# Performance work log

Measured on AMD Instinct MI355X. Metric: run time of the kernel, lower is better.

The kernel has to match this reference:

```python
import jax, jax.numpy as jnp
import numpy as np

N_NODES = 50000
N_RAND_EDGES = 800000
NEG_SLOPE = 0.2


def gat_conv(h, src, dst, W, attn_l, attn_r, bias, res_W=None, act=False):
    # DGL GATConv semantics: fc -> per-node attn halves -> per-edge leaky_relu
    # logits -> segment softmax over destination -> weighted scatter-sum.
    N = h.shape[0]
    H, D = attn_l.shape
    feat = (h @ W).reshape(N, H, D)                      # (N,H,D)
    el = (feat * attn_l[None]).sum(-1)                   # (N,H)
    er = (feat * attn_r[None]).sum(-1)                   # (N,H)
    e = jax.nn.leaky_relu(el[src] + er[dst], NEG_SLOPE)  # (E,H)
    emax = jax.ops.segment_max(e, dst, num_segments=N)   # (N,H)
    ee = jnp.exp(e - emax[dst])                          # (E,H)
    denom = jax.ops.segment_sum(ee, dst, num_segments=N)
    alpha = ee / denom[dst]                              # (E,H)
    msg = feat[src] * alpha[:, :, None]                  # (E,H,D) dominant traffic
    rst = jax.ops.segment_sum(msg, dst, num_segments=N)  # (N,H,D)
    if res_W is not None:
        rst = rst + (h @ res_W).reshape(N, H, D)
    rst = rst + bias.reshape(1, H, D)
    if act:
        rst = jax.nn.relu(rst)
    return rst


def setup_inputs() -> dict:
    key = jax.random.key(0)
    ks = jax.random.split(key, 20)
    x = jax.random.normal(ks[0], (N_NODES, 64), dtype=jnp.float32)
    src_r = jax.random.randint(ks[1], (N_RAND_EDGES,), 0, N_NODES, dtype=jnp.int32)
    dst_r = jax.random.randint(ks[2], (N_RAND_EDGES,), 0, N_NODES, dtype=jnp.int32)
    loops = jnp.arange(N_NODES, dtype=jnp.int32)
    src = jnp.concatenate([src_r, loops])   # self-loops: no zero in-degree
    dst = jnp.concatenate([dst_r, loops])
    s = 0.1
    p = lambda k, shp: jax.random.normal(k, shp, dtype=jnp.float32) * s
    return {
        "x": x, "src": src, "dst": dst,
        # layer 1: in=64 -> hid=32, heads=4, relu, no residual
        "W1": p(ks[3], (64, 128)), "al1": p(ks[4], (4, 32)), "ar1": p(ks[5], (4, 32)),
        "b1": jnp.zeros((128,), jnp.float32),
        # layer 2: in=128 -> hid=32, heads=4, relu, residual
        "W2": p(ks[6], (128, 128)), "al2": p(ks[7], (4, 32)), "ar2": p(ks[8], (4, 32)),
        "b2": jnp.zeros((128,), jnp.float32), "resW2": p(ks[9], (128, 128)),
        # layer 3: in=128 -> out=1, heads=6, no activation, residual
        "W3": p(ks[10], (128, 6)), "al3": p(ks[11], (6, 1)), "ar3": p(ks[12], (6, 1)),
        "b3": jnp.zeros((6,), jnp.float32), "resW3": p(ks[13], (128, 6)),
    }


def reference(x, src, dst, W1, al1, ar1, b1, W2, al2, ar2, b2, resW2,
              W3, al3, ar3, b3, resW3):
    h = gat_conv(x, src, dst, W1, al1, ar1, b1, None, act=True)
    h = h.reshape(h.shape[0], -1)                        # flatten heads
    h = gat_conv(h, src, dst, W2, al2, ar2, b2, resW2, act=True)
    h = h.reshape(h.shape[0], -1)
    h = gat_conv(h, src, dst, W3, al3, ar3, b3, resW3, act=False)
    return h.mean(axis=1)                                # mean over heads -> (N, out)
```

## Files before the change

### kernel.cpp

```cpp
#include <hip/hip_runtime.h>
#include <hip/hip_fp16.h>

#define NEG 0.2f
#define BUCKET_SHIFT 7
#define CAP 3200
#define PCHUNK 4096

typedef _Float16 h8 __attribute__((ext_vector_type(8)));
typedef float f4v __attribute__((ext_vector_type(4)));


__device__ __forceinline__ void wconv_dev(int bid, const float* __restrict__ W2,
                                          const float* __restrict__ rW2,
                                          float4* __restrict__ W2f,
                                          float4* __restrict__ rW2f) {
    int c = bid * 256 + threadIdx.x;
    int which = c >> 11;
    int cc = c & 2047;
    int kb = cc >> 9, rem = cc & 511, t = rem >> 6, lane = rem & 63;
    int n = (t << 4) + (lane & 15);
    int k0 = (kb << 5) + ((lane >> 4) << 3);
    const float* S = which ? rW2 : W2;
    h8 v;
#pragma unroll
    for (int i = 0; i < 8; i++) v[i] = (_Float16)S[(k0 + i) * 128 + n];
    ((h8*)(which ? rW2f : W2f))[cc] = v;
}

__device__ __forceinline__ void partition_dev(char* smem, int bid,
                                              const int* __restrict__ src,
                                              const int* __restrict__ dst,
                                              int* __restrict__ cursor,
                                              unsigned* __restrict__ part,
                                              int E, int NB) {
    unsigned* stash = (unsigned*)smem;
    int* hist = (int*)(smem + PCHUNK * 4);
    int* base = hist + 512;
    const int tid = threadIdx.x;
    const int e0 = bid * PCHUNK;

    for (int i = tid; i < NB; i += 256) hist[i] = 0;
    __syncthreads();

    for (int i = tid; i < PCHUNK; i += 256) {
        int e = e0 + i;
        unsigned pk = 0xFFFFFFFFu;
        if (e < E) {
            int d = dst[e];
            pk = ((unsigned)d << 16) | (unsigned)src[e];
            atomicAdd(&hist[d >> BUCKET_SHIFT], 1);
        }
        stash[i] = pk;
    }
    __syncthreads();

    for (int i = tid; i < NB; i += 256) {
        int hcnt = hist[i];
        base[i] = hcnt ? atomicAdd(&cursor[i], hcnt) : 0;
        hist[i] = 0;
    }
    __syncthreads();

    for (int i = tid; i < PCHUNK; i += 256) {
        unsigned pk = stash[i];
        if (pk != 0xFFFFFFFFu) {
            int b = pk >> (16 + BUCKET_SHIFT);
            int r = base[b] + atomicAdd(&hist[b], 1);
            if (r < CAP) part[(size_t)b * CAP + r] = pk;
        }
    }
}

__device__ __forceinline__ void bucket_dev(char* smem, int b,
                                           const int* __restrict__ cursor,
                                           const unsigned* __restrict__ part,
                                           int* __restrict__ csr_src,
                                           int* __restrict__ row_beg,
                                           int* __restrict__ row_end, int N) {
    int* cnt = (int*)smem;
    int* sc = cnt + 128;
    int* ex = sc + 128;
    int* cur = ex + 128;
    int* lcsr = cur + 128;
    const int tid = threadIdx.x;
    int m = cursor[b];
    m = m < CAP ? m : CAP;
    if (tid < 128) cnt[tid] = 0;
    __syncthreads();

    const unsigned* pp = part + (size_t)b * CAP;
    for (int i = tid; i < m; i += 256) atomicAdd(&cnt[(pp[i] >> 16) & 127], 1);
    __syncthreads();

    if (tid < 128) sc[tid] = cnt[tid];
    __syncthreads();
    for (int off = 1; off < 128; off <<= 1) {
        int t = (tid < 128 && tid >= off) ? sc[tid - off] : 0;
        __syncthreads();
        if (tid < 128) sc[tid] += t;
        __syncthreads();
    }
    if (tid < 128) {
        ex[tid] = sc[tid] - cnt[tid];
        cur[tid] = 0;
    }
    __syncthreads();

    for (int i = tid; i < m; i += 256) {
        unsigned pk = pp[i];
        int dlo = (pk >> 16) & 127;
        int r = atomicAdd(&cur[dlo], 1);
        lcsr[ex[dlo] + r] = (int)(pk & 0xFFFFu);
    }
    __syncthreads();

    const int gbase = b * CAP;
    for (int i = tid; i < m; i += 256) csr_src[gbase + i] = lcsr[i];
    int n = (b << BUCKET_SHIFT) + tid;
    if (tid < 128 && n < N) {
        row_beg[n] = gbase + ex[tid];
        row_end[n] = gbase + sc[tid];
    }
}

__device__ __forceinline__ void gemm_el_dev(char* smem, int bid,
                                            const float* __restrict__ A,
                                            const float* __restrict__ W,
                                            const float* __restrict__ al,
                                            const float* __restrict__ ar,
                                            __half* __restrict__ feat_h,
                                            float* __restrict__ el,
                                            float* __restrict__ er, int N) {
    constexpr int K = 64;
    float* As = (float*)smem;
    const int c = threadIdx.x & 31;
    const int rg = threadIdx.x >> 5;
    const int row0 = bid << 6;
    const int K4 = K >> 2;

    const float4* Av = (const float4*)A;
    float4* AsV = (float4*)As;
    for (int idx = threadIdx.x; idx < 16 * K; idx += 256) {
        int rr = idx / K4, kk4 = idx - rr * K4;
        int row = row0 + rr;
        float4 v = make_float4(0.f, 0.f, 0.f, 0.f);
        if (row < N) v = Av[(size_t)row * K4 + kk4];
        AsV[rr * K4 + kk4] = v;
    }
    __syncthreads();

    const float4* Wv = (const float4*)W;
    float4 acc[8];
#pragma unroll
    for (int i = 0; i < 8; i++) acc[i] = make_float4(0.f, 0.f, 0.f, 0.f);

    for (int k4 = 0; k4 < K4; k4++) {
        float4 a[8];
#pragma unroll
        for (int i = 0; i < 8; i++) a[i] = AsV[(rg * 8 + i) * K4 + k4];
#pragma unroll
        for (int kk = 0; kk < 4; kk++) {
            float4 w = Wv[((k4 << 2) + kk) * 32 + c];
#pragma unroll
            for (int i = 0; i < 8; i++) {
                float av = kk == 0 ? a[i].x : kk == 1 ? a[i].y : kk == 2 ? a[i].z : a[i].w;
                acc[i].x += av * w.x;
                acc[i].y += av * w.y;
                acc[i].z += av * w.z;
                acc[i].w += av * w.w;
            }
        }
    }

    __half2* Fh2 = (__half2*)feat_h;
#pragma unroll
    for (int i = 0; i < 8; i++) {
        int row = row0 + rg * 8 + i;
        if (row < N) {
            size_t o = ((size_t)row << 6) + (c << 1);
            Fh2[o] = __floats2half2_rn(acc[i].x, acc[i].y);
            Fh2[o + 1] = __floats2half2_rn(acc[i].z, acc[i].w);
        }
    }

    float4 alv = ((const float4*)al)[c];
    float4 arv = ((const float4*)ar)[c];
    float pel[8], per_[8];
#pragma unroll
    for (int i = 0; i < 8; i++) {
        pel[i] = acc[i].x * alv.x + acc[i].y * alv.y + acc[i].z * alv.z + acc[i].w * alv.w;
        per_[i] = acc[i].x * arv.x + acc[i].y * arv.y + acc[i].z * arv.z + acc[i].w * arv.w;
    }
#pragma unroll
    for (int m = 1; m < 8; m <<= 1) {
#pragma unroll
        for (int i = 0; i < 8; i++) {
            pel[i] += __shfl_xor(pel[i], m);
            per_[i] += __shfl_xor(per_[i], m);
        }
    }
    if ((c & 7) == 0) {
        int h = c >> 3;
#pragma unroll
        for (int i = 0; i < 8; i++) {
            int row = row0 + rg * 8 + i;
            if (row < N) {
                el[(row << 2) + h] = pel[i];
                er[(row << 2) + h] = per_[i];
            }
        }
    }
}

__global__ __launch_bounds__(256) void stage1_k(const float* __restrict__ W2,
                                                const float* __restrict__ rW2,
                                                float4* __restrict__ W2f,
                                                float4* __restrict__ rW2f,
                                                const int* __restrict__ src,
                                                const int* __restrict__ dst,
                                                int* __restrict__ cursor,
                                                unsigned* __restrict__ part,
                                                int E, int NB) {
    __shared__ __align__(16) char smem[20480];
    if (blockIdx.x < 16)
        wconv_dev(blockIdx.x, W2, rW2, W2f, rW2f);
    else
        partition_dev(smem, blockIdx.x - 16, src, dst, cursor, part, E, NB);
}

__global__ __launch_bounds__(256) void stage2_k(const int* __restrict__ cursor,
                                                const unsigned* __restrict__ part,
                                                int* __restrict__ csr_src,
                                                int* __restrict__ row_beg,
                                                int* __restrict__ row_end, int NB,
                                                const float* __restrict__ x,
                                                const float* __restrict__ W1,
                                                const float* __restrict__ al1,
                                                const float* __restrict__ ar1,
                                                __half* __restrict__ featA,
                                                float* __restrict__ el,
                                                float* __restrict__ er, int N) {
    __shared__ __align__(16) char smem[16384];
    if ((int)blockIdx.x < NB)
        bucket_dev(smem, blockIdx.x, cursor, part, csr_src, row_beg, row_end, N);
    else
        gemm_el_dev(smem, blockIdx.x - NB, x, W1, al1, ar1, featA, el, er, N);
}

#define MFMA_STAGE_AND_LOOP()                                                   \
    const int tid = threadIdx.x;                                                \
    const int row0 = blockIdx.x << 6;                                           \
    for (int i = tid; i < 2048; i += 256) WsF[i] = Wf[i];                       \
    const float4* Afv = (const float4*)A;                                       \
    for (int idx = tid; idx < 1024; idx += 256) {                               \
        int r = idx >> 4, kc = idx & 15;                                        \
        float4 v = make_float4(0.f, 0.f, 0.f, 0.f);                             \
        int row = row0 + r;                                                     \
        if (row < N) v = Afv[(size_t)row * 16 + kc];                            \
        int d = ((r >> 4) * 4 + (kc >> 2)) * 64 + (kc & 3) * 16 + (r & 15);     \
        AsF[d] = v;                                                             \
    }                                                                           \
    __syncthreads();                                                            \
    const int w = tid >> 6;                                                     \
    const int lane = tid & 63;                                                  \
    const h8* Ah = (const h8*)AsF;                                              \
    const h8* Wh = (const h8*)WsF;                                              \
    f4v acc[8];                                                                 \
    _Pragma("unroll") for (int t = 0; t < 8; t++) acc[t] = (f4v){0.f, 0.f, 0.f, 0.f}; \
    _Pragma("unroll") for (int kb = 0; kb < 4; kb++) {                          \
        h8 af = Ah[(w * 4 + kb) * 64 + lane];                                   \
        _Pragma("unroll") for (int t = 0; t < 8; t++) {                         \
            h8 bf = Wh[(kb * 8 + t) * 64 + lane];                               \
            acc[t] = __builtin_amdgcn_mfma_f32_16x16x32_f16(af, bf, acc[t], 0, 0, 0); \
        }                                                                       \
    }                                                                           \
    const int c16 = lane & 15;                                                  \
    const int rg = lane >> 4;

__global__ __launch_bounds__(256) void mfma_el_k(const _Float16* __restrict__ A,
                                                 const float4* __restrict__ Wf,
                                                 const float* __restrict__ al,
                                                 const float* __restrict__ ar,
                                                 _Float16* __restrict__ feat,
                                                 float* __restrict__ el,
                                                 float* __restrict__ er, int N) {
    __shared__ float4 WsF[2048];
    __shared__ float4 AsF[1024];
    MFMA_STAGE_AND_LOOP()

    float alv[8], arv[8];
#pragma unroll
    for (int t = 0; t < 8; t++) {
        alv[t] = al[(t << 4) + c16];
        arv[t] = ar[(t << 4) + c16];
    }
    float pel[4][4], per_[4][4];
#pragma unroll
    for (int j = 0; j < 4; j++)
#pragma unroll
        for (int hh = 0; hh < 4; hh++) {
            pel[j][hh] = acc[2 * hh][j] * alv[2 * hh] + acc[2 * hh + 1][j] * alv[2 * hh + 1];
            per_[j][hh] = acc[2 * hh][j] * arv[2 * hh] + acc[2 * hh + 1][j] * arv[2 * hh + 1];
        }
#pragma unroll
    for (int m = 1; m < 16; m <<= 1)
#pragma unroll
        for (int j = 0; j < 4; j++)
#pragma unroll
            for (int hh = 0; hh < 4; hh++) {
                pel[j][hh] += __shfl_xor(pel[j][hh], m);
                per_[j][hh] += __shfl_xor(per_[j][hh], m);
            }
    if (c16 == 0) {
#pragma unroll
        for (int j = 0; j < 4; j++) {
            int row = row0 + (w << 4) + (rg << 2) + j;
            if (row < N) {
                ((float4*)el)[row] = make_float4(pel[j][0], pel[j][1], pel[j][2], pel[j][3]);
                ((float4*)er)[row] = make_float4(per_[j][0], per_[j][1], per_[j][2], per_[j][3]);
            }
        }
    }

    _Float16* As2 = (_Float16*)AsF + (w << 11);
#pragma unroll
    for (int t = 0; t < 8; t++)
#pragma unroll
        for (int j = 0; j < 4; j++)
            As2[((rg << 2) + j) * 128 + (t << 4) + c16] = (_Float16)acc[t][j];
    __asm__ volatile("s_waitcnt lgkmcnt(0)" ::: "memory");
    const float4* As2v = (const float4*)As2;
    float4* featv = (float4*)feat;
#pragma unroll
    for (int ii = 0; ii < 4; ii++) {
        int ch = ii * 64 + lane;
        int row = row0 + (w << 4) + (ch >> 4);
        if (row < N) featv[(size_t)row * 16 + (ch & 15)] = As2v[ch];
    }
}

__global__ __launch_bounds__(256) void mfma_res_k(const _Float16* __restrict__ A,
                                                  const float4* __restrict__ Wf,
                                                  const _Float16* __restrict__ rsth,
                                                  const float* __restrict__ b2,
                                                  const float* __restrict__ W3,
                                                  const float* __restrict__ resW3,
                                                  const float* __restrict__ b3,
                                                  float* __restrict__ feat3,
                                                  float* __restrict__ res3, int N) {
    __shared__ float4 WsF[2048];
    __shared__ float4 AsF[1024];
    MFMA_STAGE_AND_LOOP()

    float4* As2v = (float4*)AsF + (w << 8);
#pragma unroll
    for (int ii = 0; ii < 4; ii++) {
        int ch = ii * 64 + lane;
        int row = row0 + (w << 4) + (ch >> 4);
        float4 v = make_float4(0.f, 0.f, 0.f, 0.f);
        if (row < N) v = ((const float4*)rsth)[(size_t)row * 16 + (ch & 15)];
        As2v[ch] = v;
    }
    __asm__ volatile("s_waitcnt lgkmcnt(0)" ::: "memory");
    const _Float16* As2 = (const _Float16*)As2v;

    float b2v[8];
#pragma unroll
    for (int t = 0; t < 8; t++) b2v[t] = b2[(t << 4) + c16];

    float hv[8][4];
#pragma unroll
    for (int t = 0; t < 8; t++)
#pragma unroll
        for (int j = 0; j < 4; j++) {
            float rv = (float)As2[((rg << 2) + j) * 128 + (t << 4) + c16];
            hv[t][j] = fmaxf(acc[t][j] + rv + b2v[t], 0.f);
        }

    float f3[4][6], r3[4][6];
#pragma unroll
    for (int j = 0; j < 4; j++)
#pragma unroll
        for (int h = 0; h < 6; h++) {
            f3[j][h] = 0.f;
            r3[j][h] = 0.f;
        }
#pragma unroll
    for (int t = 0; t < 8; t++) {
        int col = (t << 4) + c16;
        const float* w3p = W3 + col * 6;
        const float* rwp = resW3 + col * 6;
#pragma unroll
        for (int h = 0; h < 6; h++) {
            float w3 = w3p[h], rw = rwp[h];
#pragma unroll
            for (int j = 0; j < 4; j++) {
                f3[j][h] = fmaf(hv[t][j], w3, f3[j][h]);
                r3[j][h] = fmaf(hv[t][j], rw, r3[j][h]);
            }
        }
    }
#pragma unroll
    for (int m = 1; m < 16; m <<= 1)
#pragma unroll
        for (int j = 0; j < 4; j++)
#pragma unroll
            for (int h = 0; h < 6; h++) {
                f3[j][h] += __shfl_xor(f3[j][h], m);
                r3[j][h] += __shfl_xor(r3[j][h], m);
            }
    if (c16 == 0) {
#pragma unroll
        for (int j = 0; j < 4; j++) {
            int row = row0 + (w << 4) + (rg << 2) + j;
            if (row < N) {
#pragma unroll
                for (int h = 0; h < 6; h++) {
                    feat3[row * 6 + h] = f3[j][h];
                    res3[row * 6 + h] = r3[j][h] + b3[h];
                }
            }
        }
    }
}

template <bool BR>
__global__ __launch_bounds__(256) void pull2_k(const int* __restrict__ row_beg,
                                               const int* __restrict__ row_end,
                                               const int* __restrict__ csr_src,
                                               const float* __restrict__ el,
                                               const float* __restrict__ er,
                                               const __half* __restrict__ feat_h,
                                               const float* __restrict__ bias,
                                               __half* __restrict__ outp, int N) {
    int n = (blockIdx.x << 2) + (threadIdx.x >> 6);
    if (n >= N) return;
    unsigned l = threadIdx.x & 63;
    unsigned h = l >> 4;
    float erd = er[((unsigned)n << 2) + h];
    const __half2* feat2 = (const __half2*)feat_h;
    int beg = __builtin_amdgcn_readfirstlane(row_beg[n]);
    int end = __builtin_amdgcn_readfirstlane(row_end[n]);
    float ax = 0.f, ay = 0.f, den = 0.f;
    int p = beg;
    for (; p + 4 <= end; p += 4) {
        int s0 = csr_src[p], s1 = csr_src[p + 1];
        int s2 = csr_src[p + 2], s3 = csr_src[p + 3];
        float e0 = el[((unsigned)s0 << 2) + h];
        float e1 = el[((unsigned)s1 << 2) + h];
        float e2 = el[((unsigned)s2 << 2) + h];
        float e3 = el[((unsigned)s3 << 2) + h];
        __half2 g0 = feat2[((unsigned)s0 << 6) + l];
        __half2 g1 = feat2[((unsigned)s1 << 6) + l];
        __half2 g2 = feat2[((unsigned)s2 << 6) + l];
        __half2 g3 = feat2[((unsigned)s3 << 6) + l];
        float x0 = e0 + erd, x1 = e1 + erd, x2 = e2 + erd, x3 = e3 + erd;
        x0 = fmaxf(x0, NEG * x0);
        x1 = fmaxf(x1, NEG * x1);
        x2 = fmaxf(x2, NEG * x2);
        x3 = fmaxf(x3, NEG * x3);
        float w0 = __expf(x0), w1 = __expf(x1), w2 = __expf(x2), w3 = __expf(x3);
        float2 f0 = __half22float2(g0), f1 = __half22float2(g1);
        float2 f2 = __half22float2(g2), f3 = __half22float2(g3);
        den += (w0 + w1) + (w2 + w3);
        ax = fmaf(w0, f0.x, ax);
        ay = fmaf(w0, f0.y, ay);
        ax = fmaf(w1, f1.x, ax);
        ay = fmaf(w1, f1.y, ay);
        ax = fmaf(w2, f2.x, ax);
        ay = fmaf(w2, f2.y, ay);
        ax = fmaf(w3, f3.x, ax);
        ay = fmaf(w3, f3.y, ay);
    }
    for (; p < end; p++) {
        int s0 = csr_src[p];
        float e0 = el[((unsigned)s0 << 2) + h];
        __half2 g0 = feat2[((unsigned)s0 << 6) + l];
        float x0 = e0 + erd;
        x0 = fmaxf(x0, NEG * x0);
        float w0 = __expf(x0);
        float2 f0 = __half22float2(g0);
        den += w0;
        ax = fmaf(w0, f0.x, ax);
        ay = fmaf(w0, f0.y, ay);
    }
    float inv = 1.f / den;
    float vx = ax * inv, vy = ay * inv;
    if (BR) {
        float2 b = ((const float2*)bias)[l];
        vx = fmaxf(vx + b.x, 0.f);
        vy = fmaxf(vy + b.y, 0.f);
    }
    ((__half2*)outp)[((size_t)n << 6) + l] = __floats2half2_rn(vx, vy);
}

__global__ __launch_bounds__(256) void pull6f_k(const int* __restrict__ row_beg,
                                                const int* __restrict__ row_end,
                                                const int* __restrict__ csr_src,
                                                const float* __restrict__ feat3,
                                                const float* __restrict__ al3,
                                                const float* __restrict__ ar3,
                                                const float* __restrict__ res3,
                                                float* __restrict__ out, int N) {
    int n = blockIdx.x * blockDim.x + threadIdx.x;
    if (n >= N) return;
    float a3[6], fdr[6], acc[6], den[6];
#pragma unroll
    for (int h = 0; h < 6; h++) {
        a3[h] = al3[h];
        fdr[h] = feat3[n * 6 + h] * ar3[h];
        acc[h] = 0.f;
        den[h] = 0.f;
    }
    int beg = row_beg[n], end = row_end[n];
    for (int p = beg; p < end; p++) {
        int s = csr_src[p];
#pragma unroll
        for (int h = 0; h < 6; h++) {
            float f = feat3[(unsigned)s * 6 + h];
            float x = fmaf(f, a3[h], fdr[h]);
            x = fmaxf(x, NEG * x);
            float w = __expf(x);
            den[h] += w;
            acc[h] = fmaf(w, f, acc[h]);
        }
    }
    float m = 0.f;
#pragma unroll
    for (int h = 0; h < 6; h++) m += acc[h] / den[h] + res3[n * 6 + h];
    out[n] = m * (1.f / 6.f);
}

extern "C" void kernel_launch(void* const* d_in, const int* in_sizes, int n_in,
                              void* d_out, int out_size, void* d_ws, size_t ws_size,
                              hipStream_t stream) {
    const float* x = (const float*)d_in[0];
    const int* src = (const int*)d_in[1];
    const int* dst = (const int*)d_in[2];
    const float* W1 = (const float*)d_in[3];
    const float* al1 = (const float*)d_in[4];
    const float* ar1 = (const float*)d_in[5];
    const float* b1 = (const float*)d_in[6];
    const float* W2 = (const float*)d_in[7];
    const float* al2 = (const float*)d_in[8];
    const float* ar2 = (const float*)d_in[9];
    const float* b2 = (const float*)d_in[10];
    const float* resW2 = (const float*)d_in[11];
    const float* W3 = (const float*)d_in[12];
    const float* al3 = (const float*)d_in[13];
    const float* ar3 = (const float*)d_in[14];
    const float* b3 = (const float*)d_in[15];
    const float* resW3 = (const float*)d_in[16];
    float* out = (float*)d_out;

    const int N = in_sizes[0] / 64;
    const int E = in_sizes[1];
    const int NB = (N + 127) >> BUCKET_SHIFT;

    float* ws = (float*)d_ws;
    __half* featA = (__half*)ws;
    __half* h2h = (__half*)(ws + (size_t)N * 64);
    __half* rsth = (__half*)(ws + (size_t)N * 128);
    float* el = ws + (size_t)N * 192;
    float* er = el + (size_t)N * 4;
    float* feat3 = el;
    float* res3 = ws + (size_t)N * 200;
    float* W2f = res3 + (size_t)N * 6;
    float* rW2f = W2f + 8192;
    int* ip = (int*)(rW2f + 8192);
    int* cursor = ip;
    int* row_beg = cursor + 512;
    int* row_end = row_beg + N;
    unsigned* part = (unsigned*)(row_end + N);
    int* csr_src = (int*)(part + (size_t)NB * CAP);

    const int gN = (N + 255) / 256;
    const int gN64 = (N + 63) / 64;
    const int gNw = (N + 3) / 4;
    const int gP = (E + PCHUNK - 1) / PCHUNK;

    hipMemsetAsync(cursor, 0, sizeof(int) * 512, stream);
    stage1_k<<<16 + gP, 256, 0, stream>>>(W2, resW2, (float4*)W2f, (float4*)rW2f,
                                          src, dst, cursor, part, E, NB);
    stage2_k<<<NB + gN64, 256, 0, stream>>>(cursor, part, csr_src, row_beg, row_end,
                                            NB, x, W1, al1, ar1, featA, el, er, N);

    pull2_k<true><<<gNw, 256, 0, stream>>>(row_beg, row_end, csr_src, el, er,
                                           featA, b1, h2h, N);

    mfma_el_k<<<gN64, 256, 0, stream>>>((const _Float16*)h2h, (const float4*)W2f,
                                        al2, ar2, (_Float16*)featA, el, er, N);
    pull2_k<false><<<gNw, 256, 0, stream>>>(row_beg, row_end, csr_src, el, er,
                                            featA, nullptr, rsth, N);
    mfma_res_k<<<gN64, 256, 0, stream>>>((const _Float16*)h2h, (const float4*)rW2f,
                                         (const _Float16*)rsth, b2, W3, resW3, b3,
                                         feat3, res3, N);

    pull6f_k<<<gN, 256, 0, stream>>>(row_beg, row_end, csr_src, feat3, al3, ar3,
                                     res3, out, N);
}
```

Measured before the change: 253.7 us.

## Use half-wave per node with 8-byte gathers; pad layer-3 features for float4 loads

pull2_k now maps each destination node to 32 lanes instead of 64, so one wavefront serves two nodes. Each lane gathers four fp16 features with a single 8-byte load and issues half as many el loads and exp calls per feature, which raises memory-level parallelism. Layer-3 features are stored with a stride of 8 floats so pull6f_k can fetch each source row with two float4 loads instead of six scalar loads. The trade-off is that the two nodes in a wavefront can have different degrees, causing loop divergence, and the row bounds are no longer wave-uniform scalars.

```diff
diff --git a/kernel.cpp b/kernel.cpp
--- a/kernel.cpp
+++ b/kernel.cpp
@@ -416,7 +416,7 @@
             if (row < N) {
 #pragma unroll
                 for (int h = 0; h < 6; h++) {
-                    feat3[row * 6 + h] = f3[j][h];
+                    feat3[(size_t)row * 8 + h] = f3[j][h];
                     res3[row * 6 + h] = r3[j][h] + b3[h];
                 }
             }
@@ -433,15 +433,14 @@
                                                const __half* __restrict__ feat_h,
                                                const float* __restrict__ bias,
                                                __half* __restrict__ outp, int N) {
-    int n = (blockIdx.x << 2) + (threadIdx.x >> 6);
+    int n = (blockIdx.x << 3) + (threadIdx.x >> 5);
     if (n >= N) return;
-    unsigned l = threadIdx.x & 63;
-    unsigned h = l >> 4;
+    unsigned q = threadIdx.x & 31;
+    unsigned h = q >> 3;
     float erd = er[((unsigned)n << 2) + h];
-    const __half2* feat2 = (const __half2*)feat_h;
-    int beg = __builtin_amdgcn_readfirstlane(row_beg[n]);
-    int end = __builtin_amdgcn_readfirstlane(row_end[n]);
-    float ax = 0.f, ay = 0.f, den = 0.f;
+    const uint2* feat4 = (const uint2*)feat_h;
+    int beg = row_beg[n], end = row_end[n];
+    float a0 = 0.f, a1 = 0.f, a2 = 0.f, a3 = 0.f, den = 0.f;
     int p = beg;
     for (; p + 4 <= end; p += 4) {
         int s0 = csr_src[p], s1 = csr_src[p + 1];
@@ -450,48 +449,73 @@
         float e1 = el[((unsigned)s1 << 2) + h];
         float e2 = el[((unsigned)s2 << 2) + h];
         float e3 = el[((unsigned)s3 << 2) + h];
-        __half2 g0 = feat2[((unsigned)s0 << 6) + l];
-        __half2 g1 = feat2[((unsigned)s1 << 6) + l];
-        __half2 g2 = feat2[((unsigned)s2 << 6) + l];
-        __half2 g3 = feat2[((unsigned)s3 << 6) + l];
+        uint2 g0 = feat4[((unsigned)s0 << 5) + q];
+        uint2 g1 = feat4[((unsigned)s1 << 5) + q];
+        uint2 g2 = feat4[((unsigned)s2 << 5) + q];
+        uint2 g3 = feat4[((unsigned)s3 << 5) + q];
         float x0 = e0 + erd, x1 = e1 + erd, x2 = e2 + erd, x3 = e3 + erd;
         x0 = fmaxf(x0, NEG * x0);
         x1 = fmaxf(x1, NEG * x1);
         x2 = fmaxf(x2, NEG * x2);
         x3 = fmaxf(x3, NEG * x3);
         float w0 = __expf(x0), w1 = __expf(x1), w2 = __expf(x2), w3 = __expf(x3);
-        float2 f0 = __half22float2(g0), f1 = __half22float2(g1);
-        float2 f2 = __half22float2(g2), f3 = __half22float2(g3);
         den += (w0 + w1) + (w2 + w3);
-        ax = fmaf(w0, f0.x, ax);
-        ay = fmaf(w0, f0.y, ay);
-        ax = fmaf(w1, f1.x, ax);
-        ay = fmaf(w1, f1.y, ay);
-        ax = fmaf(w2, f2.x, ax);
-        ay = fmaf(w2, f2.y, ay);
-        ax = fmaf(w3, f3.x, ax);
-        ay = fmaf(w3, f3.y, ay);
+        float2 lo, hi;
+        lo = __half22float2(*(__half2*)&g0.x);
+        hi = __half22float2(*(__half2*)&g0.y);
+        a0 = fmaf(w0, lo.x, a0);
+        a1 = fmaf(w0, lo.y, a1);
+        a2 = fmaf(w0, hi.x, a2);
+        a3 = fmaf(w0, hi.y, a3);
+        lo = __half22float2(*(__half2*)&g1.x);
+        hi = __half22float2(*(__half2*)&g1.y);
+        a0 = fmaf(w1, lo.x, a0);
+        a1 = fmaf(w1, lo.y, a1);
+        a2 = fmaf(w1, hi.x, a2);
+        a3 = fmaf(w1, hi.y, a3);
+        lo = __half22float2(*(__half2*)&g2.x);
+        hi = __half22float2(*(__half2*)&g2.y);
+        a0 = fmaf(w2, lo.x, a0);
+        a1 = fmaf(w2, lo.y, a1);
+        a2 = fmaf(w2, hi.x, a2);
+        a3 = fmaf(w2, hi.y, a3);
+        lo = __half22float2(*(__half2*)&g3.x);
+        hi = __half22float2(*(__half2*)&g3.y);
+        a0 = fmaf(w3, lo.x, a0);
+        a1 = fmaf(w3, lo.y, a1);
+        a2 = fmaf(w3, hi.x, a2);
+        a3 = fmaf(w3, hi.y, a3);
     }
     for (; p < end; p++) {
         int s0 = csr_src[p];
         float e0 = el[((unsigned)s0 << 2) + h];
-        __half2 g0 = feat2[((unsigned)s0 << 6) + l];
+        uint2 g0 = feat4[((unsigned)s0 << 5) + q];
         float x0 = e0 + erd;
         x0 = fmaxf(x0, NEG * x0);
         float w0 = __expf(x0);
-        float2 f0 = __half22float2(g0);
         den += w0;
-        ax = fmaf(w0, f0.x, ax);
-        ay = fmaf(w0, f0.y, ay);
+        float2 lo = __half22float2(*(__half2*)&g0.x);
+        float2 hi = __half22float2(*(__half2*)&g0.y);
+        a0 = fmaf(w0, lo.x, a0);
+        a1 = fmaf(w0, lo.y, a1);
+        a2 = fmaf(w0, hi.x, a2);
+        a3 = fmaf(w0, hi.y, a3);
     }
     float inv = 1.f / den;
-    float vx = ax * inv, vy = ay * inv;
+    float v0 = a0 * inv, v1 = a1 * inv, v2 = a2 * inv, v3 = a3 * inv;
     if (BR) {
-        float2 b = ((const float2*)bias)[l];
-        vx = fmaxf(vx + b.x, 0.f);
-        vy = fmaxf(vy + b.y, 0.f);
-    }
-    ((__half2*)outp)[((size_t)n << 6) + l] = __floats2half2_rn(vx, vy);
+        float4 bv = ((const float4*)bias)[q];
+        v0 = fmaxf(v0 + bv.x, 0.f);
+        v1 = fmaxf(v1 + bv.y, 0.f);
+        v2 = fmaxf(v2 + bv.z, 0.f);
+        v3 = fmaxf(v3 + bv.w, 0.f);
+    }
+    __half2 o01 = __floats2half2_rn(v0, v1);
+    __half2 o23 = __floats2half2_rn(v2, v3);
+    uint2 st;
+    st.x = *(unsigned*)&o01;
+    st.y = *(unsigned*)&o23;
+    ((uint2*)outp)[((size_t)n << 5) + q] = st;
 }
 
 __global__ __launch_bounds__(256) void pull6f_k(const int* __restrict__ row_beg,
@@ -504,25 +528,28 @@
                                                 float* __restrict__ out, int N) {
     int n = blockIdx.x * blockDim.x + threadIdx.x;
     if (n >= N) return;
+    const float4* f4p = (const float4*)feat3;
     float a3[6], fdr[6], acc[6], den[6];
 #pragma unroll
     for (int h = 0; h < 6; h++) {
         a3[h] = al3[h];
-        fdr[h] = feat3[n * 6 + h] * ar3[h];
+        fdr[h] = feat3[(size_t)n * 8 + h] * ar3[h];
         acc[h] = 0.f;
         den[h] = 0.f;
     }
     int beg = row_beg[n], end = row_end[n];
     for (int p = beg; p < end; p++) {
         int s = csr_src[p];
+        float4 fa = f4p[(size_t)s * 2];
+        float4 fb = f4p[(size_t)s * 2 + 1];
+        float f[6] = {fa.x, fa.y, fa.z, fa.w, fb.x, fb.y};
 #pragma unroll
         for (int h = 0; h < 6; h++) {
-            float f = feat3[(unsigned)s * 6 + h];
-            float x = fmaf(f, a3[h], fdr[h]);
+            float x = fmaf(f[h], a3[h], fdr[h]);
             x = fmaxf(x, NEG * x);
             float w = __expf(x);
             den[h] += w;
-            acc[h] = fmaf(w, f, acc[h]);
+            acc[h] = fmaf(w, f[h], acc[h]);
         }
     }
     float m = 0.f;
@@ -576,7 +603,7 @@
 
     const int gN = (N + 255) / 256;
     const int gN64 = (N + 63) / 64;
-    const int gNw = (N + 3) / 4;
+    const int gNw8 = (N + 7) / 8;
     const int gP = (E + PCHUNK - 1) / PCHUNK;
 
     hipMemsetAsync(cursor, 0, sizeof(int) * 512, stream);
@@ -585,13 +612,13 @@
     stage2_k<<<NB + gN64, 256, 0, stream>>>(cursor, part, csr_src, row_beg, row_end,
                                             NB, x, W1, al1, ar1, featA, el, er, N);
 
-    pull2_k<true><<<gNw, 256, 0, stream>>>(row_beg, row_end, csr_src, el, er,
-                                           featA, b1, h2h, N);
+    pull2_k<true><<<gNw8, 256, 0, stream>>>(row_beg, row_end, csr_src, el, er,
+                                            featA, b1, h2h, N);
 
     mfma_el_k<<<gN64, 256, 0, stream>>>((const _Float16*)h2h, (const float4*)W2f,
                                         al2, ar2, (_Float16*)featA, el, er, N);
-    pull2_k<false><<<gNw, 256, 0, stream>>>(row_beg, row_end, csr_src, el, er,
-                                            featA, nullptr, rsth, N);
+    pull2_k<false><<<gNw8, 256, 0, stream>>>(row_beg, row_end, csr_src, el, er,
+                                             featA, nullptr, rsth, N);
     mfma_res_k<<<gN64, 256, 0, stream>>>((const _Float16*)h2h, (const float4*)rW2f,
                                          (const _Float16*)rsth, b2, W3, resW3, b3,
                                          feat3, res3, N);
```

After: 256.7 us. No clear change (+1.2%).
